# Kernel tuning notes

Measured on AMD Instinct MI355X. Metric: run time of the kernel, lower is better.

The kernel has to match this reference:

```python
import jax, jax.numpy as jnp
import numpy as np

D_MODEL = 1024
HEADS = 16
D_KEY = D_MODEL // HEADS


def setup_inputs() -> dict:
    key = jax.random.key(0)
    ks = jax.random.split(key, 7)
    B, S = 4, 2048
    queries = jax.random.normal(ks[0], (B, S, D_MODEL), dtype=jnp.float32)
    keys = jax.random.normal(ks[1], (B, S, D_MODEL), dtype=jnp.float32)
    values = jax.random.normal(ks[2], (B, S, D_MODEL), dtype=jnp.float32)
    scale = 1.0 / np.sqrt(D_MODEL)
    # Per-head projection weights, torch Linear layout [out=d_key, in=d_model], stacked over heads
    Wq = jax.random.uniform(ks[3], (HEADS, D_KEY, D_MODEL), jnp.float32, -scale, scale)
    Wk = jax.random.uniform(ks[4], (HEADS, D_KEY, D_MODEL), jnp.float32, -scale, scale)
    Wv = jax.random.uniform(ks[5], (HEADS, D_KEY, D_MODEL), jnp.float32, -scale, scale)
    Wo = jax.random.uniform(ks[6], (D_MODEL, D_MODEL), jnp.float32, -scale, scale)
    return {"queries": queries, "keys": keys, "values": values,
            "Wq": Wq, "Wk": Wk, "Wv": Wv, "Wo": Wo}


def reference(queries, keys, values, Wq, Wk, Wv, Wo):
    # Project per head: [B,S,D] x [H,K,D] -> [B,H,S,K]
    q = jnp.einsum('bsd,hkd->bhsk', queries, Wq)
    k = jnp.einsum('bsd,hkd->bhsk', keys, Wk)
    v = jnp.einsum('bsd,hkd->bhsk', values, Wv)
    attn = jnp.einsum('bhqk,bhsk->bhqs', q, k) / jnp.sqrt(jnp.float32(D_KEY))
    attn = jax.nn.softmax(attn, axis=-1)
    out = jnp.einsum('bhqs,bhsk->bhqk', attn, v)  # [B,H,S,K]
    B, H, S, K = out.shape
    # concat heads along last dim (head order = torch cat order)
    out = out.transpose(0, 2, 1, 3).reshape(B, S, H * K)
    return out @ Wo.T
```

## Files before the change

### kernel.cpp

```cpp
#include <hip/hip_runtime.h>
#include <hip/hip_bf16.h>

typedef __attribute__((ext_vector_type(8))) short short8;
typedef __attribute__((ext_vector_type(4))) short short4v;
typedef __attribute__((ext_vector_type(4))) float f32x4;
typedef __bf16 bf16x8 __attribute__((ext_vector_type(8)));

#define DEVI static __device__ __forceinline__

DEVI short f2bs(float f) {
    union { __hip_bfloat16 h; short s; } u;
    u.h = __float2bfloat16(f);
    return u.s;
}

DEVI f32x4 mfma16(short8 a, short8 b, f32x4 c) {
    return __builtin_amdgcn_mfma_f32_16x16x32_bf16(
        __builtin_bit_cast(bf16x8, a), __builtin_bit_cast(bf16x8, b), c, 0, 0, 0);
}

DEVI void glds16(const short* g, short* l) {
    __builtin_amdgcn_global_load_lds((const __attribute__((address_space(1))) void*)g,
                                     (__attribute__((address_space(3))) void*)l, 16, 0, 0);
}

__global__ __launch_bounds__(256) void cvt_all(const float4* __restrict__ q,
                                               const float4* __restrict__ k,
                                               const float4* __restrict__ v,
                                               const float4* __restrict__ wq,
                                               const float4* __restrict__ wk,
                                               const float4* __restrict__ wv,
                                               const float4* __restrict__ wo,
                                               short4v* __restrict__ dq,
                                               short4v* __restrict__ dk,
                                               short4v* __restrict__ dv,
                                               short4v* __restrict__ dwq,
                                               short4v* __restrict__ dwk,
                                               short4v* __restrict__ dwv,
                                               short4v* __restrict__ dwo) {
    int bid = blockIdx.x;
    float4 x;
    short4v s;
    if (bid < 8192) {
        int i = bid * 256 + threadIdx.x;
        x = q[i]; s.x = f2bs(x.x); s.y = f2bs(x.y); s.z = f2bs(x.z); s.w = f2bs(x.w); dq[i] = s;
        x = k[i]; s.x = f2bs(x.x); s.y = f2bs(x.y); s.z = f2bs(x.z); s.w = f2bs(x.w); dk[i] = s;
        x = v[i]; s.x = f2bs(x.x); s.y = f2bs(x.y); s.z = f2bs(x.z); s.w = f2bs(x.w); dv[i] = s;
    } else {
        int i = (bid - 8192) * 256 + threadIdx.x;
        x = wq[i]; s.x = f2bs(x.x); s.y = f2bs(x.y); s.z = f2bs(x.z); s.w = f2bs(x.w); dwq[i] = s;
        x = wk[i]; s.x = f2bs(x.x); s.y = f2bs(x.y); s.z = f2bs(x.z); s.w = f2bs(x.w); dwk[i] = s;
        x = wv[i]; s.x = f2bs(x.x); s.y = f2bs(x.y); s.z = f2bs(x.z); s.w = f2bs(x.w); dwv[i] = s;
        x = wo[i]; s.x = f2bs(x.x); s.y = f2bs(x.y); s.z = f2bs(x.z); s.w = f2bs(x.w); dwo[i] = s;
    }
}

template <typename EpiT>
DEVI void gemm_body(const short* A, const short* Bw, short* smem, int m0, int n0, EpiT epi) {
    short* As = smem;
    short* Bs = smem + 8192;
    const int t = threadIdx.x;
    const int lane = t & 63, w = t >> 6;
    const int col = lane & 15, quad = lane >> 4;
    const int wm = (w & 1) * 64, wn = (w >> 1) * 64;

    f32x4 acc[4][4];
#pragma unroll
    for (int i = 0; i < 4; ++i)
#pragma unroll
        for (int j = 0; j < 4; ++j) acc[i][j] = (f32x4){0.f, 0.f, 0.f, 0.f};

    for (int kt = 0; kt < 16; ++kt) {
        const int k0 = kt * 64;
#pragma unroll
        for (int j = 0; j < 4; ++j) {
            int cbase = (j * 4 + w) * 64;
            int c = cbase + lane;
            int row = c >> 3, kc = (c & 7) ^ (row & 7);
            glds16(A + (size_t)(m0 + row) * 1024 + k0 + kc * 8, As + cbase * 8);
        }
#pragma unroll
        for (int j = 0; j < 4; ++j) {
            int cbase = (j * 4 + w) * 64;
            int c = cbase + lane;
            int row = c >> 3, kc = (c & 7) ^ (row & 7);
            glds16(Bw + (size_t)(n0 + row) * 1024 + k0 + kc * 8, Bs + cbase * 8);
        }
        __syncthreads();
#pragma unroll
        for (int ks = 0; ks < 2; ++ks) {
            short8 a[4], b[4];
#pragma unroll
            for (int i = 0; i < 4; ++i) {
                int row = wm + i * 16 + col;
                int kc = (ks * 4 + quad) ^ (col & 7);
                a[i] = *(const short8*)(As + (row * 8 + kc) * 8);
            }
#pragma unroll
            for (int i = 0; i < 4; ++i) {
                int row = wn + i * 16 + col;
                int kc = (ks * 4 + quad) ^ (col & 7);
                b[i] = *(const short8*)(Bs + (row * 8 + kc) * 8);
            }
#pragma unroll
            for (int mi = 0; mi < 4; ++mi)
#pragma unroll
                for (int ni = 0; ni < 4; ++ni)
                    acc[mi][ni] = mfma16(a[mi], b[ni], acc[mi][ni]);
        }
        __syncthreads();
    }
    epi(acc, wm, wn, col, quad);
}

__global__ __launch_bounds__(256) void qkv_gemm(const short* __restrict__ xq,
                                                const short* __restrict__ xk,
                                                const short* __restrict__ xv,
                                                const short* __restrict__ wq,
                                                const short* __restrict__ wk,
                                                const short* __restrict__ wv,
                                                short* __restrict__ qp,
                                                short* __restrict__ kp,
                                                short* __restrict__ vpt, float qscale) {
    __shared__ __align__(16) short smem[17408];
    const int z = blockIdx.z;
    const int m0 = blockIdx.y * 128, n0 = blockIdx.x * 128;
    const short* A = (z == 0) ? xq : (z == 1) ? xk : xv;
    const short* W = (z == 0) ? wq : (z == 1) ? wk : wv;

    if (z < 2) {
        short* outs = (z == 0) ? qp : kp;
        const float scale = (z == 0) ? qscale : 1.0f;
        gemm_body(A, W, smem, m0, n0, [&](f32x4 (&acc)[4][4], int wm, int wn, int col, int quad) {
            short* T = smem;
#pragma unroll
            for (int mi = 0; mi < 4; ++mi)
#pragma unroll
                for (int ni = 0; ni < 4; ++ni)
#pragma unroll
                    for (int r = 0; r < 4; ++r)
                        T[(wm + mi * 16 + quad * 4 + r) * 136 + wn + ni * 16 + col] =
                            f2bs(acc[mi][ni][r] * scale);
            __syncthreads();
            int t = threadIdx.x;
            int ml = t >> 1, nh = (t & 1) * 64;
            int m = m0 + ml;
            int b = m >> 11, s = m & 2047;
#pragma unroll
            for (int j = 0; j < 8; ++j) {
                int n = n0 + nh + j * 8;
                short8 vv = *(const short8*)(T + ml * 136 + nh + j * 8);
                size_t off = ((size_t)(b * 16 + (n >> 6)) * 2048 + s) * 64 + (n & 63);
                *(short8*)(outs + off) = vv;
            }
        });
    } else {
        gemm_body(A, W, smem, m0, n0, [&](f32x4 (&acc)[4][4], int wm, int wn, int col, int quad) {
            short* T = smem;
#pragma unroll
            for (int mi = 0; mi < 4; ++mi)
#pragma unroll
                for (int ni = 0; ni < 4; ++ni) {
                    int n_l = wn + ni * 16 + col;
                    int m_l = wm + mi * 16 + quad * 4;
                    short4v sv;
                    sv.x = f2bs(acc[mi][ni][0]); sv.y = f2bs(acc[mi][ni][1]);
                    sv.z = f2bs(acc[mi][ni][2]); sv.w = f2bs(acc[mi][ni][3]);
                    *(short4v*)(T + n_l * 132 + m_l) = sv;
                }
            __syncthreads();
            int t = threadIdx.x;
            int nrow = t >> 1, mh = (t & 1) * 64;
            int b = m0 >> 11, s0 = m0 & 2047;
            size_t base = ((size_t)(b * 1024 + n0 + nrow)) * 2048 + s0 + mh;
#pragma unroll
            for (int j = 0; j < 16; ++j) {
                unsigned long long vv = *(const unsigned long long*)(T + nrow * 132 + mh + j * 4);
                *(unsigned long long*)(vpt + base + j * 4) = vv;
            }
        });
    }
}

__global__ __launch_bounds__(256) void out_gemm(const short* __restrict__ ao,
                                                const short* __restrict__ wo,
                                                float* __restrict__ outf) {
    __shared__ __align__(16) short smem[16896];
    const int m0 = blockIdx.y * 128, n0 = blockIdx.x * 128;
    gemm_body(ao, wo, smem, m0, n0, [&](f32x4 (&acc)[4][4], int wm, int wn, int col, int quad) {
#pragma unroll
        for (int mi = 0; mi < 4; ++mi)
#pragma unroll
            for (int ni = 0; ni < 4; ++ni)
#pragma unroll
                for (int r = 0; r < 4; ++r) {
                    int m = m0 + wm + mi * 16 + quad * 4 + r;
                    int n = n0 + wn + ni * 16 + col;
                    outf[(size_t)m * 1024 + n] = acc[mi][ni][r];
                }
    });
}

__global__ __launch_bounds__(256, 4) void flash_attn(const short* __restrict__ qp,
                                                     const short* __restrict__ kp,
                                                     const short* __restrict__ vpt,
                                                     short* __restrict__ ao) {
    __shared__ __align__(16) short smem[8192 + 8192 + 4096];
    short* Ks = smem;
    short* Vs = smem + 8192;

    const int t = threadIdx.x, lane = t & 63, w = t >> 6;
    const int col = lane & 15, quad = lane >> 4;
    const int bh = blockIdx.x, q0 = blockIdx.y * 128;
    const short* qb = qp + (size_t)bh * 2048 * 64;
    const short* kb = kp + (size_t)bh * 2048 * 64;
    const short* vb = vpt + (size_t)bh * 64 * 2048;
    short* Pw = smem + 16384 + w * 1024;

#pragma unroll
    for (int j = 0; j < 4; ++j) {
        int cbase = (j * 4 + w) * 64;
        int c = cbase + lane;
        int row = c >> 3, kc = (c & 7) ^ (row & 7);
        glds16(qb + (size_t)(q0 + row) * 64 + kc * 8, Ks + cbase * 8);
    }
    __syncthreads();
    short8 bQ[2][2];
#pragma unroll
    for (int qi = 0; qi < 2; ++qi)
#pragma unroll
        for (int ks = 0; ks < 2; ++ks) {
            int row = w * 32 + qi * 16 + col;
            int kc = (ks * 4 + quad) ^ (col & 7);
            bQ[qi][ks] = *(const short8*)(Ks + (row * 8 + kc) * 8);
        }
    __syncthreads();

    f32x4 acc_o[2][4];
    float l_r[2] = {0.f, 0.f};
#pragma unroll
    for (int qi = 0; qi < 2; ++qi)
#pragma unroll
        for (int ni = 0; ni < 4; ++ni) acc_o[qi][ni] = (f32x4){0.f, 0.f, 0.f, 0.f};

    for (int kt = 0; kt < 16; ++kt) {
#pragma unroll
        for (int j = 0; j < 4; ++j) {
            int cbase = (j * 4 + w) * 64;
            int c = cbase + lane;
            int row = c >> 3, kc = (c & 7) ^ (row & 7);
            glds16(kb + (size_t)(kt * 128 + row) * 64 + kc * 8, Ks + cbase * 8);
        }
#pragma unroll
        for (int j = 0; j < 4; ++j) {
            int m = w * 4 + j;
            int dk = m * 4 + (lane >> 4);
            int sc = (lane & 15) ^ (dk & 15);
            glds16(vb + (size_t)dk * 2048 + kt * 128 + sc * 8, Vs + m * 512);
        }
        __syncthreads();

#pragma unroll
        for (int g = 0; g < 4; ++g) {
#pragma unroll
            for (int h = 0; h < 2; ++h) {
                int kei = g * 2 + h;
                f32x4 st[2];
                st[0] = (f32x4){0.f, 0.f, 0.f, 0.f};
                st[1] = (f32x4){0.f, 0.f, 0.f, 0.f};
#pragma unroll
                for (int ks = 0; ks < 2; ++ks) {
                    int row = kei * 16 + col;
                    int kc = (ks * 4 + quad) ^ (col & 7);
                    short8 aK = *(const short8*)(Ks + (row * 8 + kc) * 8);
#pragma unroll
                    for (int qi = 0; qi < 2; ++qi) st[qi] = mfma16(aK, bQ[qi][ks], st[qi]);
                }
#pragma unroll
                for (int qi = 0; qi < 2; ++qi) {
                    float p0 = __builtin_amdgcn_exp2f(st[qi][0]);
                    float p1 = __builtin_amdgcn_exp2f(st[qi][1]);
                    float p2 = __builtin_amdgcn_exp2f(st[qi][2]);
                    float p3 = __builtin_amdgcn_exp2f(st[qi][3]);
                    l_r[qi] += (p0 + p1) + (p2 + p3);
                    short4v pv;
                    pv.x = f2bs(p0); pv.y = f2bs(p1); pv.z = f2bs(p2); pv.w = f2bs(p3);
                    int row = qi * 16 + col;
                    int ch = (h * 2 + (quad >> 1)) ^ (row & 3);
                    *(short4v*)(Pw + row * 32 + ch * 8 + (quad & 1) * 4) = pv;
                }
            }
            short8 pa[2];
#pragma unroll
            for (int qi = 0; qi < 2; ++qi) {
                int row = qi * 16 + col;
                pa[qi] = *(const short8*)(Pw + row * 32 + (quad ^ (row & 3)) * 8);
            }
#pragma unroll
            for (int ni = 0; ni < 4; ++ni) {
                int dk = ni * 16 + col;
                short8 bv = *(const short8*)(Vs + dk * 128 + (((g * 4 + quad) ^ col) * 8));
#pragma unroll
                for (int qi = 0; qi < 2; ++qi)
                    acc_o[qi][ni] = mfma16(pa[qi], bv, acc_o[qi][ni]);
            }
        }
        __syncthreads();
    }

#pragma unroll
    for (int qi = 0; qi < 2; ++qi) {
        l_r[qi] += __shfl_xor(l_r[qi], 16);
        l_r[qi] += __shfl_xor(l_r[qi], 32);
    }
    const int b = bh >> 4, hd = bh & 15;
#pragma unroll
    for (int qi = 0; qi < 2; ++qi)
#pragma unroll
        for (int r = 0; r < 4; ++r) {
            float lq = __shfl(l_r[qi], quad * 4 + r);
            float inv = 1.0f / lq;
            int q = q0 + w * 32 + qi * 16 + quad * 4 + r;
#pragma unroll
            for (int ni = 0; ni < 4; ++ni)
                ao[((size_t)(b * 2048 + q)) * 1024 + hd * 64 + ni * 16 + col] =
                    f2bs(acc_o[qi][ni][r] * inv);
        }
}

extern "C" void kernel_launch(void* const* d_in, const int* in_sizes, int n_in,
                              void* d_out, int out_size, void* d_ws, size_t ws_size,
                              hipStream_t stream) {
    const float* q  = (const float*)d_in[0];
    const float* k  = (const float*)d_in[1];
    const float* v  = (const float*)d_in[2];
    const float* Wq = (const float*)d_in[3];
    const float* Wk = (const float*)d_in[4];
    const float* Wv = (const float*)d_in[5];
    const float* Wo = (const float*)d_in[6];
    float* out = (float*)d_out;

    short* ws = (short*)d_ws;
    const size_t SZ = (size_t)64 * 2048 * 64;
    const size_t WZ = (size_t)1024 * 1024;
    short* xq  = ws;
    short* xk  = ws + SZ;
    short* xv  = ws + 2 * SZ;
    short* qp  = ws + 3 * SZ;
    short* kp  = ws + 4 * SZ;
    short* wqb = ws + 5 * SZ;
    short* wkb = wqb + WZ;
    short* wvb = wqb + 2 * WZ;
    short* wob = wqb + 3 * WZ;
    short* ao  = xq;
    short* vpt = xk;

    const float QSCALE = 0.125f * 1.44269504088896f;

    cvt_all<<<dim3(9216), dim3(256), 0, stream>>>(
        (const float4*)q, (const float4*)k, (const float4*)v, (const float4*)Wq,
        (const float4*)Wk, (const float4*)Wv, (const float4*)Wo, (short4v*)xq, (short4v*)xk,
        (short4v*)xv, (short4v*)wqb, (short4v*)wkb, (short4v*)wvb, (short4v*)wob);
    dim3 blk(256);
    qkv_gemm<<<dim3(8, 64, 3), blk, 0, stream>>>(xq, xk, xv, wqb, wkb, wvb, qp, kp, vpt, QSCALE);
    flash_attn<<<dim3(64, 16), blk, 0, stream>>>(qp, kp, vpt, ao);
    out_gemm<<<dim3(8, 64), blk, 0, stream>>>(ao, wob, out);
}
```

Baseline: 346.3 us.

## Switch flash attention to 32x32 MFMA with register-shuffled P operand

Rewrites the attention inner loop to use 32x32x16 bf16 MFMA tiles instead of 16x16x32. It computes S^T so each lane holds one query row's probabilities, then builds the PV A-operand through a cross-half lane shuffle instead of a round trip through LDS. This drops the per-wave P scratch buffer and its LDS writes and reads, and shrinks shared memory. In exchange it adds shuffles and select logic, raises accumulator register pressure, and moves the final normalization to per-element lane shuffles.

```diff
diff --git a/kernel.cpp b/kernel.cpp
--- a/kernel.cpp
+++ b/kernel.cpp
@@ -4,6 +4,7 @@
 typedef __attribute__((ext_vector_type(8))) short short8;
 typedef __attribute__((ext_vector_type(4))) short short4v;
 typedef __attribute__((ext_vector_type(4))) float f32x4;
+typedef __attribute__((ext_vector_type(16))) float f32x16;
 typedef __bf16 bf16x8 __attribute__((ext_vector_type(8)));
 
 #define DEVI static __device__ __forceinline__
@@ -14,8 +15,19 @@
     return u.s;
 }
 
+DEVI unsigned pk2(float a, float b) {
+    unsigned lo = (unsigned short)f2bs(a);
+    unsigned hi = (unsigned short)f2bs(b);
+    return lo | (hi << 16);
+}
+
 DEVI f32x4 mfma16(short8 a, short8 b, f32x4 c) {
     return __builtin_amdgcn_mfma_f32_16x16x32_bf16(
+        __builtin_bit_cast(bf16x8, a), __builtin_bit_cast(bf16x8, b), c, 0, 0, 0);
+}
+
+DEVI f32x16 mfma32(short8 a, short8 b, f32x16 c) {
+    return __builtin_amdgcn_mfma_f32_32x32x16_bf16(
         __builtin_bit_cast(bf16x8, a), __builtin_bit_cast(bf16x8, b), c, 0, 0, 0);
 }
 
@@ -205,17 +217,16 @@
                                                      const short* __restrict__ kp,
                                                      const short* __restrict__ vpt,
                                                      short* __restrict__ ao) {
-    __shared__ __align__(16) short smem[8192 + 8192 + 4096];
+    __shared__ __align__(16) short smem[16384];
     short* Ks = smem;
     short* Vs = smem + 8192;
 
     const int t = threadIdx.x, lane = t & 63, w = t >> 6;
-    const int col = lane & 15, quad = lane >> 4;
+    const int l31 = lane & 31, half = lane >> 5;
     const int bh = blockIdx.x, q0 = blockIdx.y * 128;
     const short* qb = qp + (size_t)bh * 2048 * 64;
     const short* kb = kp + (size_t)bh * 2048 * 64;
     const short* vb = vpt + (size_t)bh * 64 * 2048;
-    short* Pw = smem + 16384 + w * 1024;
 
 #pragma unroll
     for (int j = 0; j < 4; ++j) {
@@ -225,23 +236,19 @@
         glds16(qb + (size_t)(q0 + row) * 64 + kc * 8, Ks + cbase * 8);
     }
     __syncthreads();
-    short8 bQ[2][2];
-#pragma unroll
-    for (int qi = 0; qi < 2; ++qi)
-#pragma unroll
-        for (int ks = 0; ks < 2; ++ks) {
-            int row = w * 32 + qi * 16 + col;
-            int kc = (ks * 4 + quad) ^ (col & 7);
-            bQ[qi][ks] = *(const short8*)(Ks + (row * 8 + kc) * 8);
-        }
+    short8 bQ[4];
+    {
+        int row = w * 32 + l31;
+#pragma unroll
+        for (int ks = 0; ks < 4; ++ks) {
+            int kc = (ks * 2 + half) ^ (row & 7);
+            bQ[ks] = *(const short8*)(Ks + (row * 8 + kc) * 8);
+        }
+    }
     __syncthreads();
 
-    f32x4 acc_o[2][4];
-    float l_r[2] = {0.f, 0.f};
-#pragma unroll
-    for (int qi = 0; qi < 2; ++qi)
-#pragma unroll
-        for (int ni = 0; ni < 4; ++ni) acc_o[qi][ni] = (f32x4){0.f, 0.f, 0.f, 0.f};
+    f32x16 acc[2] = {};
+    float l_r = 0.f;
 
     for (int kt = 0; kt < 16; ++kt) {
 #pragma unroll
@@ -261,70 +268,62 @@
         __syncthreads();
 
 #pragma unroll
-        for (int g = 0; g < 4; ++g) {
-#pragma unroll
-            for (int h = 0; h < 2; ++h) {
-                int kei = g * 2 + h;
-                f32x4 st[2];
-                st[0] = (f32x4){0.f, 0.f, 0.f, 0.f};
-                st[1] = (f32x4){0.f, 0.f, 0.f, 0.f};
-#pragma unroll
-                for (int ks = 0; ks < 2; ++ks) {
-                    int row = kei * 16 + col;
-                    int kc = (ks * 4 + quad) ^ (col & 7);
+        for (int sub = 0; sub < 4; ++sub) {
+            f32x16 st = {};
+            {
+                int row = sub * 32 + l31;
+#pragma unroll
+                for (int ks = 0; ks < 4; ++ks) {
+                    int kc = (ks * 2 + half) ^ (row & 7);
                     short8 aK = *(const short8*)(Ks + (row * 8 + kc) * 8);
-#pragma unroll
-                    for (int qi = 0; qi < 2; ++qi) st[qi] = mfma16(aK, bQ[qi][ks], st[qi]);
+                    st = mfma32(aK, bQ[ks], st);
                 }
-#pragma unroll
-                for (int qi = 0; qi < 2; ++qi) {
-                    float p0 = __builtin_amdgcn_exp2f(st[qi][0]);
-                    float p1 = __builtin_amdgcn_exp2f(st[qi][1]);
-                    float p2 = __builtin_amdgcn_exp2f(st[qi][2]);
-                    float p3 = __builtin_amdgcn_exp2f(st[qi][3]);
-                    l_r[qi] += (p0 + p1) + (p2 + p3);
-                    short4v pv;
-                    pv.x = f2bs(p0); pv.y = f2bs(p1); pv.z = f2bs(p2); pv.w = f2bs(p3);
-                    int row = qi * 16 + col;
-                    int ch = (h * 2 + (quad >> 1)) ^ (row & 3);
-                    *(short4v*)(Pw + row * 32 + ch * 8 + (quad & 1) * 4) = pv;
+            }
+            unsigned u[8], x[8];
+#pragma unroll
+            for (int j = 0; j < 8; ++j) {
+                float p0 = __builtin_amdgcn_exp2f(st[2 * j]);
+                float p1 = __builtin_amdgcn_exp2f(st[2 * j + 1]);
+                l_r += p0 + p1;
+                u[j] = pk2(p0, p1);
+            }
+#pragma unroll
+            for (int j = 0; j < 8; ++j) x[j] = __shfl_xor(u[j], 32);
+            union U4 { unsigned u[4]; short8 s; } fa, fb;
+            fa.u[0] = half ? x[2] : u[0];
+            fa.u[1] = half ? x[3] : u[1];
+            fa.u[2] = half ? u[2] : x[0];
+            fa.u[3] = half ? u[3] : x[1];
+            fb.u[0] = half ? x[6] : u[4];
+            fb.u[1] = half ? x[7] : u[5];
+            fb.u[2] = half ? u[6] : x[4];
+            fb.u[3] = half ? u[7] : x[5];
+#pragma unroll
+            for (int nb = 0; nb < 2; ++nb) {
+                int dk = nb * 32 + l31;
+#pragma unroll
+                for (int kset = 0; kset < 2; ++kset) {
+                    int kc = (sub * 4 + kset * 2 + half) ^ (dk & 15);
+                    short8 bv = *(const short8*)(Vs + dk * 128 + kc * 8);
+                    acc[nb] = mfma32(kset ? fb.s : fa.s, bv, acc[nb]);
                 }
             }
-            short8 pa[2];
-#pragma unroll
-            for (int qi = 0; qi < 2; ++qi) {
-                int row = qi * 16 + col;
-                pa[qi] = *(const short8*)(Pw + row * 32 + (quad ^ (row & 3)) * 8);
-            }
-#pragma unroll
-            for (int ni = 0; ni < 4; ++ni) {
-                int dk = ni * 16 + col;
-                short8 bv = *(const short8*)(Vs + dk * 128 + (((g * 4 + quad) ^ col) * 8));
-#pragma unroll
-                for (int qi = 0; qi < 2; ++qi)
-                    acc_o[qi][ni] = mfma16(pa[qi], bv, acc_o[qi][ni]);
-            }
         }
         __syncthreads();
     }
 
-#pragma unroll
-    for (int qi = 0; qi < 2; ++qi) {
-        l_r[qi] += __shfl_xor(l_r[qi], 16);
-        l_r[qi] += __shfl_xor(l_r[qi], 32);
-    }
+    l_r += __shfl_xor(l_r, 32);
+    float inv = 1.0f / l_r;
     const int b = bh >> 4, hd = bh & 15;
 #pragma unroll
-    for (int qi = 0; qi < 2; ++qi)
-#pragma unroll
-        for (int r = 0; r < 4; ++r) {
-            float lq = __shfl(l_r[qi], quad * 4 + r);
-            float inv = 1.0f / lq;
-            int q = q0 + w * 32 + qi * 16 + quad * 4 + r;
-#pragma unroll
-            for (int ni = 0; ni < 4; ++ni)
-                ao[((size_t)(b * 2048 + q)) * 1024 + hd * 64 + ni * 16 + col] =
-                    f2bs(acc_o[qi][ni][r] * inv);
+    for (int nb = 0; nb < 2; ++nb)
+#pragma unroll
+        for (int j = 0; j < 16; ++j) {
+            int m = (j & 3) + 8 * (j >> 2) + 4 * half;
+            float iq = __shfl(inv, m);
+            int q = q0 + w * 32 + m;
+            ao[((size_t)(b * 2048 + q)) * 1024 + hd * 64 + nb * 32 + l31] =
+                f2bs(acc[nb][j] * iq);
         }
 }
 
```

Result: slower. 359.4 us (+3.8%).
